# Optimization experiments

Measured on AMD Instinct MI355X. Metric: run time of the kernel, lower is better.

The kernel has to match this reference:

```python
import jax, jax.numpy as jnp
import numpy as np

V, E, H, S, B = 32000, 512, 1024, 32, 32


def setup_inputs() -> dict:
    key = jax.random.key(0)
    ks = jax.random.split(key, 16)
    s = 0.05
    return {
        "word": jax.random.randint(ks[0], (B,), 0, V),
        "seq": jax.random.randint(ks[1], (S, B), 0, V),
        "emb": jax.random.normal(ks[2], (V, E), jnp.float32) * s,
        "Wl": jax.random.normal(ks[3], (H, E), jnp.float32) * s,
        "bl": jnp.zeros((H,), jnp.float32),
        "Wih": jax.random.normal(ks[4], (4 * H, E), jnp.float32) * s,
        "Whh": jax.random.normal(ks[5], (4 * H, H), jnp.float32) * s,
        "bih": jnp.zeros((4 * H,), jnp.float32),
        "bhh": jnp.zeros((4 * H,), jnp.float32),
        "Wz": jax.random.normal(ks[6], (H, E + H), jnp.float32) * s,
        "bz": jnp.zeros((H,), jnp.float32),
        "Wr": jax.random.normal(ks[7], (E, E + H), jnp.float32) * s,
        "br": jnp.zeros((E,), jnp.float32),
        "Wh": jax.random.normal(ks[8], (H, E + H), jnp.float32) * s,
        "bh": jnp.zeros((H,), jnp.float32),
        "Wo": jax.random.normal(ks[9], (V, H), jnp.float32) * s,
        "bo": jnp.zeros((V,), jnp.float32),
    }


def reference(word, seq, emb, Wl, bl, Wih, Whh, bih, bhh, Wz, bz, Wr, br, Wh, bh, Wo, bo):
    we = emb[word]              # [B, E] defined-word embedding (constant per step)
    se = emb[seq]               # [S, B, E] definition token embeddings
    h0 = we @ Wl.T + bl         # word_linear init: hidden = (h0, h0)

    def step(carry, x):
        h, c = carry
        # torch LSTMCell: gate order i, f, g, o
        gates = x @ Wih.T + h @ Whh.T + (bih + bhh)
        i, f, g, o = jnp.split(gates, 4, axis=-1)
        c = jax.nn.sigmoid(f) * c + jax.nn.sigmoid(i) * jnp.tanh(g)
        h = jax.nn.sigmoid(o) * jnp.tanh(c)
        # GRU-style g-gating with the defined-word embedding
        inp_h = jnp.concatenate([we, h], axis=-1)           # [B, E+H]
        z = jax.nn.sigmoid(inp_h @ Wz.T + bz)               # [B, H]
        r = jax.nn.sigmoid(inp_h @ Wr.T + br)               # [B, E]
        hc = jnp.concatenate([r * we, h], axis=-1)          # [B, E+H]
        hh = jnp.tanh(hc @ Wh.T + bh)
        h = (1.0 - z) * h + z * hh
        return (h, c), h

    (hf, cf), hs = jax.lax.scan(step, (h0, h0), se)
    out = hs @ Wo.T + bo        # [S, B, V] logits (dropout p=0 -> identity)
    return out, hf, cf
```

## Files before the change

kernel.cpp:

```cpp
#include <hip/hip_runtime.h>


typedef __bf16 bf16;
typedef __bf16 bf16x8 __attribute__((ext_vector_type(8)));
typedef __bf16 bf16x4v __attribute__((ext_vector_type(4)));
typedef float f32x4 __attribute__((ext_vector_type(4)));
typedef unsigned long long u64;
typedef unsigned int u32;

#define Vv 32000
#define Ee 512
#define Hh 1024
#define Ss 32
#define Bb 32
#define KC 1536

#define MFMA16(a, b, c) __builtin_amdgcn_mfma_f32_16x16x32_bf16(a, b, c, 0, 0, 0)

static __device__ __forceinline__ float sigf(float x) { return 1.0f / (1.0f + __expf(-x)); }

static __device__ __forceinline__ u64 cload_u64(const void* p) {
  return __hip_atomic_load((const u64*)p, __ATOMIC_RELAXED, __HIP_MEMORY_SCOPE_SYSTEM);
}
static __device__ __forceinline__ void cstore_u64(void* p, u64 v) {
  __hip_atomic_store((u64*)p, v, __ATOMIC_RELAXED, __HIP_MEMORY_SCOPE_SYSTEM);
}
static __device__ __forceinline__ void cstore_u32(void* p, u32 v) {
  __hip_atomic_store((u32*)p, v, __ATOMIC_RELAXED, __HIP_MEMORY_SCOPE_SYSTEM);
}
static __device__ __forceinline__ bf16x8 cload_bf8(const bf16* p) {
  union { u64 w[2]; bf16x8 v; } u;
  u.w[0] = cload_u64(p);
  u.w[1] = cload_u64(p + 4);
  return u.v;
}
union F2U64 { float f[2]; u64 u; };
union B2U32 { bf16 h[2]; u32 u; };


__global__ void k_conv_gates(const float* __restrict__ Wih, const float* __restrict__ Whh,
                             const float* __restrict__ bih, const float* __restrict__ bhh,
                             bf16* __restrict__ Wgh, bf16* __restrict__ Wgl,
                             float* __restrict__ bg) {
  int g = blockIdx.y;
  int col = blockIdx.x * 256 + threadIdx.x;
  int k = g >> 2, s = g & 3;
  int src = s * Hh + k;
  float v = (col < Ee) ? Wih[(size_t)src * Ee + col] : Whh[(size_t)src * Hh + (col - Ee)];
  bf16 h = (bf16)v;
  Wgh[(size_t)g * KC + col] = h;
  Wgl[(size_t)g * KC + col] = (bf16)(v - (float)h);
  if (col == 0) bg[g] = bih[src] + bhh[src];
}

__global__ void k_conv_zr2(const float* __restrict__ Wz, const float* __restrict__ Wr,
                           bf16* __restrict__ W2h, bf16* __restrict__ W2l) {
  int j = blockIdx.y;
  int col = blockIdx.x * 256 + threadIdx.x;
  float v = (j < Hh) ? Wz[(size_t)j * KC + Ee + col] : Wr[(size_t)(j - Hh) * KC + Ee + col];
  bf16 h = (bf16)v;
  W2h[(size_t)j * Hh + col] = h;
  W2l[(size_t)j * Hh + col] = (bf16)(v - (float)h);
}

__global__ void k_conv_wh(const float* __restrict__ A, bf16* __restrict__ hi,
                          bf16* __restrict__ lo) {
  int j = blockIdx.y;
  int k = blockIdx.x * 256 + threadIdx.x;
  float v = A[(size_t)j * KC + k];
  bf16 h = (bf16)v;
  hi[(size_t)j * KC + k] = h;
  lo[(size_t)j * KC + k] = (bf16)(v - (float)h);
}


__global__ void k_gather_we(const int* __restrict__ word, const float* __restrict__ emb,
                            float* __restrict__ we) {
  int b = blockIdx.y;
  int e = blockIdx.x * 256 + threadIdx.x;
  we[b * Ee + e] = emb[(size_t)word[b] * Ee + e];
}

__global__ void k_gather_se(const int* __restrict__ seq, const float* __restrict__ emb,
                            bf16* __restrict__ se_h, bf16* __restrict__ se_l) {
  int tb = blockIdx.y;
  int e = blockIdx.x * 256 + threadIdx.x;
  float v = emb[(size_t)seq[tb] * Ee + e];
  bf16 h = (bf16)v;
  se_h[(size_t)tb * Ee + e] = h;
  se_l[(size_t)tb * Ee + e] = (bf16)(v - (float)h);
}

__global__ void k_init_h0(const float* __restrict__ we, const float* __restrict__ Wl,
                          const float* __restrict__ bl, float* __restrict__ c,
                          bf16* __restrict__ h_h, bf16* __restrict__ h_l) {
  int o = blockIdx.x * 4 + (threadIdx.x >> 6);
  int lane = threadIdx.x & 63;
  int b = o >> 10, n = o & 1023;
  const float* wr = we + b * Ee;
  const float* wl = Wl + (size_t)n * Ee;
  int e0 = lane * 8;
  float4 a0 = *(const float4*)(wr + e0);
  float4 a1 = *(const float4*)(wr + e0 + 4);
  float4 b0 = *(const float4*)(wl + e0);
  float4 b1 = *(const float4*)(wl + e0 + 4);
  float s = a0.x * b0.x + a0.y * b0.y + a0.z * b0.z + a0.w * b0.w +
            a1.x * b1.x + a1.y * b1.y + a1.z * b1.z + a1.w * b1.w;
  for (int off = 32; off; off >>= 1) s += __shfl_down(s, off);
  if (lane == 0) {
    s += bl[n];
    c[o] = s;
    bf16 h = (bf16)s;
    h_h[o] = h;
    h_l[o] = (bf16)(s - (float)h);
  }
}

__global__ __launch_bounds__(256) void k_zrwe(const float* __restrict__ we,
                                              const float* __restrict__ Wz,
                                              const float* __restrict__ Wr,
                                              const float* __restrict__ bz,
                                              const float* __restrict__ br,
                                              float* __restrict__ zrwe) {
  int tid = threadIdx.x;
  int w = tid >> 6, lane = tid & 63, l16 = lane & 15, quad = lane >> 4;
  int j0 = (blockIdx.x * 4 + w) * 16;
  int j = j0 + l16;
  const float* wrow = (j < Hh) ? (Wz + (size_t)j * KC) : (Wr + (size_t)(j - Hh) * KC);
  f32x4 acc[2];
  acc[0] = (f32x4){0.f, 0.f, 0.f, 0.f};
  acc[1] = (f32x4){0.f, 0.f, 0.f, 0.f};
  for (int kk = 0; kk < Ee; kk += 32) {
    bf16x8 bh, bl;
#pragma unroll
    for (int i = 0; i < 8; ++i) {
      float v = wrow[kk + quad * 8 + i];
      bf16 hv = (bf16)v;
      bh[i] = hv;
      bl[i] = (bf16)(v - (float)hv);
    }
#pragma unroll
    for (int mt = 0; mt < 2; ++mt) {
      bf16x8 ah, al;
      const float* arow = we + (size_t)(mt * 16 + l16) * Ee + kk + quad * 8;
#pragma unroll
      for (int i = 0; i < 8; ++i) {
        float v = arow[i];
        bf16 hv = (bf16)v;
        ah[i] = hv;
        al[i] = (bf16)(v - (float)hv);
      }
      acc[mt] = MFMA16(ah, bh, acc[mt]);
      acc[mt] = MFMA16(al, bh, acc[mt]);
      acc[mt] = MFMA16(ah, bl, acc[mt]);
    }
  }
  float bias = (j < Hh) ? bz[j] : br[j - Hh];
#pragma unroll
  for (int mt = 0; mt < 2; ++mt)
#pragma unroll
    for (int r = 0; r < 4; ++r) {
      int b = mt * 16 + quad * 4 + r;
      zrwe[b * KC + j] = acc[mt][r] + bias;
    }
}


struct RecurArgs {
  const bf16 *Wgh, *Wgl;
  const bf16 *W2h, *W2l;
  const bf16 *Whh2, *Whl2;
  const bf16 *seh, *sel;
  const float *bg;
  const float *bhb;
  const float *zrwe;
  const float *we;
  bf16 *h_h, *h_l;
  float *c, *hl, *z, *hf;
  bf16 *hlh, *hll;
  bf16 *rweh, *rwel;
  bf16 *hs;
  unsigned *bar;
};

static __device__ __forceinline__ void gridbar(unsigned* bar, unsigned n) {
  asm volatile("s_waitcnt vmcnt(0)" ::: "memory");
  __syncthreads();
  if (threadIdx.x == 0) {
    unsigned v = __hip_atomic_fetch_add(bar, 1u, __ATOMIC_RELAXED, __HIP_MEMORY_SCOPE_AGENT);
    if (v == n * 256u - 1u) {
      __hip_atomic_store(bar + 64, n, __ATOMIC_RELAXED, __HIP_MEMORY_SCOPE_AGENT);
    } else {
      while ((int)(__hip_atomic_fetch_add(bar + 64, 0u, __ATOMIC_RELAXED,
                                          __HIP_MEMORY_SCOPE_AGENT) -
                   n) < 0)
        __builtin_amdgcn_s_sleep(4);
    }
  }
  __syncthreads();
}

__global__ __launch_bounds__(512) void k_recur(RecurArgs a) {
  __shared__ __align__(16) bf16 sWa[2][16 * 1024];
  __shared__ __align__(16) bf16 sWx[2][16 * 1024];
  __shared__ float red[8][32][17];

  int blk = blockIdx.x, tid = threadIdx.x;
  int w = tid >> 6, lane = tid & 63, l16 = lane & 15, quad = lane >> 4;

  for (int i = tid; i < 2048; i += 512) {
    int row = i >> 7, ch = i & 127, e = ch * 8;
    int d = row * 1024 + (e ^ ((row & 7) << 3));
    *(bf16x8*)&sWa[0][d] = *(const bf16x8*)&a.Wgh[(size_t)(blk * 16 + row) * KC + Ee + e];
    *(bf16x8*)&sWa[1][d] = *(const bf16x8*)&a.Wgl[(size_t)(blk * 16 + row) * KC + Ee + e];
    if (blk < 96) {
      *(bf16x8*)&sWx[0][d] = *(const bf16x8*)&a.W2h[(size_t)(blk * 16 + row) * Hh + e];
      *(bf16x8*)&sWx[1][d] = *(const bf16x8*)&a.W2l[(size_t)(blk * 16 + row) * Hh + e];
    } else if (blk < 160) {
      *(bf16x8*)&sWx[0][d] =
          *(const bf16x8*)&a.Whh2[(size_t)((blk - 96) * 16 + row) * KC + Ee + e];
      *(bf16x8*)&sWx[1][d] =
          *(const bf16x8*)&a.Whl2[(size_t)((blk - 96) * 16 + row) * KC + Ee + e];
    }
  }
  __syncthreads();

  unsigned bcnt = 0;

  for (int t = 0; t < Ss; ++t) {
    {
      f32x4 acc[2];
      acc[0] = (f32x4){0.f, 0.f, 0.f, 0.f};
      acc[1] = (f32x4){0.f, 0.f, 0.f, 0.f};
#pragma unroll
      for (int it = 0; it < 6; ++it) {
        int kk = w * 192 + it * 32;
        bf16x8 bh, bl;
        if (kk < Ee) {
          bh = *(const bf16x8*)&a.Wgh[(size_t)(blk * 16 + l16) * KC + kk + quad * 8];
          bl = *(const bf16x8*)&a.Wgl[(size_t)(blk * 16 + l16) * KC + kk + quad * 8];
        } else {
          int eo = (kk - Ee) + quad * 8;
          int d = l16 * 1024 + (eo ^ ((l16 & 7) << 3));
          bh = *(const bf16x8*)&sWa[0][d];
          bl = *(const bf16x8*)&sWa[1][d];
        }
#pragma unroll
        for (int mt = 0; mt < 2; ++mt) {
          int bb = mt * 16 + l16;
          bf16x8 ah, al;
          if (kk < Ee) {
            ah = *(const bf16x8*)&a.seh[(size_t)(t * Bb + bb) * Ee + kk + quad * 8];
            al = *(const bf16x8*)&a.sel[(size_t)(t * Bb + bb) * Ee + kk + quad * 8];
          } else {
            ah = cload_bf8(&a.h_h[(size_t)bb * Hh + (kk - Ee) + quad * 8]);
            al = cload_bf8(&a.h_l[(size_t)bb * Hh + (kk - Ee) + quad * 8]);
          }
          acc[mt] = MFMA16(ah, bh, acc[mt]);
          acc[mt] = MFMA16(al, bh, acc[mt]);
          acc[mt] = MFMA16(ah, bl, acc[mt]);
        }
      }
#pragma unroll
      for (int mt = 0; mt < 2; ++mt)
#pragma unroll
        for (int r = 0; r < 4; ++r) red[w][mt * 16 + quad * 4 + r][l16] = acc[mt][r];
    }
    __syncthreads();
    if (tid < 64) {
      int bb = tid >> 1, kl0 = (tid & 1) * 2;
      B2U32 ph, pl;
      F2U64 phl;
#pragma unroll
      for (int u2 = 0; u2 < 2; ++u2) {
        int kl = kl0 + u2;
        float g4[4];
#pragma unroll
        for (int s = 0; s < 4; ++s) {
          int jl = kl * 4 + s;
          float sum = a.bg[blk * 16 + jl];
#pragma unroll
          for (int w2 = 0; w2 < 8; ++w2) sum += red[w2][bb][jl];
          g4[s] = sum;
        }
        int idx = bb * Hh + blk * 4 + kl;
        float cn = sigf(g4[1]) * a.c[idx] + sigf(g4[0]) * tanhf(g4[2]);
        float hvv = sigf(g4[3]) * tanhf(cn);
        a.c[idx] = cn;
        phl.f[u2] = hvv;
        bf16 hb = (bf16)hvv;
        ph.h[u2] = hb;
        pl.h[u2] = (bf16)(hvv - (float)hb);
      }
      int base = bb * Hh + blk * 4 + kl0;
      cstore_u64(&a.hl[base], phl.u);
      cstore_u32(&a.hlh[base], ph.u);
      cstore_u32(&a.hll[base], pl.u);
    }
    gridbar(a.bar, ++bcnt);

    if (blk < 96) {
      f32x4 acc[2];
      acc[0] = (f32x4){0.f, 0.f, 0.f, 0.f};
      acc[1] = (f32x4){0.f, 0.f, 0.f, 0.f};
#pragma unroll
      for (int it = 0; it < 4; ++it) {
        int kk = w * 128 + it * 32;
        int eo = kk + quad * 8;
        int d = l16 * 1024 + (eo ^ ((l16 & 7) << 3));
        bf16x8 bh = *(const bf16x8*)&sWx[0][d];
        bf16x8 bl = *(const bf16x8*)&sWx[1][d];
#pragma unroll
        for (int mt = 0; mt < 2; ++mt) {
          int bb = mt * 16 + l16;
          bf16x8 ah = cload_bf8(&a.hlh[(size_t)bb * Hh + kk + quad * 8]);
          bf16x8 al = cload_bf8(&a.hll[(size_t)bb * Hh + kk + quad * 8]);
          acc[mt] = MFMA16(ah, bh, acc[mt]);
          acc[mt] = MFMA16(al, bh, acc[mt]);
          acc[mt] = MFMA16(ah, bl, acc[mt]);
        }
      }
#pragma unroll
      for (int mt = 0; mt < 2; ++mt)
#pragma unroll
        for (int r = 0; r < 4; ++r) red[w][mt * 16 + quad * 4 + r][l16] = acc[mt][r];
      __syncthreads();
      if (tid < 256) {
        int bb = tid >> 3, jl0 = (tid & 7) * 2;
        float v[2];
#pragma unroll
        for (int u2 = 0; u2 < 2; ++u2) {
          int jl = jl0 + u2;
          int j = blk * 16 + jl;
          float s = a.zrwe[bb * KC + j];
#pragma unroll
          for (int w2 = 0; w2 < 8; ++w2) s += red[w2][bb][jl];
          v[u2] = s;
        }
        int j = blk * 16 + jl0;
        if (blk < 64) {
          F2U64 pz;
          pz.f[0] = sigf(v[0]);
          pz.f[1] = sigf(v[1]);
          cstore_u64(&a.z[bb * Hh + j], pz.u);
        } else {
          int e = j - Hh;
          B2U32 ph, pl;
#pragma unroll
          for (int u2 = 0; u2 < 2; ++u2) {
            float rv = sigf(v[u2]) * a.we[bb * Ee + e + u2];
            bf16 hb = (bf16)rv;
            ph.h[u2] = hb;
            pl.h[u2] = (bf16)(rv - (float)hb);
          }
          cstore_u32(&a.rweh[bb * Ee + e], ph.u);
          cstore_u32(&a.rwel[bb * Ee + e], pl.u);
        }
      }
    }
    gridbar(a.bar, ++bcnt);

    if (blk >= 96 && blk < 160) {
      int j0 = (blk - 96) * 16;
      f32x4 acc[2];
      acc[0] = (f32x4){0.f, 0.f, 0.f, 0.f};
      acc[1] = (f32x4){0.f, 0.f, 0.f, 0.f};
#pragma unroll
      for (int it = 0; it < 6; ++it) {
        int kk = w * 192 + it * 32;
        bf16x8 bh, bl;
        if (kk < Ee) {
          bh = *(const bf16x8*)&a.Whh2[(size_t)(j0 + l16) * KC + kk + quad * 8];
          bl = *(const bf16x8*)&a.Whl2[(size_t)(j0 + l16) * KC + kk + quad * 8];
        } else {
          int eo = (kk - Ee) + quad * 8;
          int d = l16 * 1024 + (eo ^ ((l16 & 7) << 3));
          bh = *(const bf16x8*)&sWx[0][d];
          bl = *(const bf16x8*)&sWx[1][d];
        }
#pragma unroll
        for (int mt = 0; mt < 2; ++mt) {
          int bb = mt * 16 + l16;
          bf16x8 ah, al;
          if (kk < Ee) {
            ah = cload_bf8(&a.rweh[(size_t)bb * Ee + kk + quad * 8]);
            al = cload_bf8(&a.rwel[(size_t)bb * Ee + kk + quad * 8]);
          } else {
            ah = cload_bf8(&a.hlh[(size_t)bb * Hh + (kk - Ee) + quad * 8]);
            al = cload_bf8(&a.hll[(size_t)bb * Hh + (kk - Ee) + quad * 8]);
          }
          acc[mt] = MFMA16(ah, bh, acc[mt]);
          acc[mt] = MFMA16(al, bh, acc[mt]);
          acc[mt] = MFMA16(ah, bl, acc[mt]);
        }
      }
#pragma unroll
      for (int mt = 0; mt < 2; ++mt)
#pragma unroll
        for (int r = 0; r < 4; ++r) red[w][mt * 16 + quad * 4 + r][l16] = acc[mt][r];
      __syncthreads();
      if (tid < 256) {
        int bb = tid >> 3, jl0 = (tid & 7) * 2;
        int j = j0 + jl0;
        F2U64 hlp, zp;
        hlp.u = cload_u64(&a.hl[bb * Hh + j]);
        zp.u = cload_u64(&a.z[bb * Hh + j]);
        B2U32 ph, pl, phs;
        float hf2[2];
#pragma unroll
        for (int u2 = 0; u2 < 2; ++u2) {
          int jl = jl0 + u2;
          float s = a.bhb[j + u2];
#pragma unroll
          for (int w2 = 0; w2 < 8; ++w2) s += red[w2][bb][jl];
          float hhv = tanhf(s);
          float hn = (1.f - zp.f[u2]) * hlp.f[u2] + zp.f[u2] * hhv;
          hf2[u2] = hn;
          bf16 hb = (bf16)hn;
          ph.h[u2] = hb;
          pl.h[u2] = (bf16)(hn - (float)hb);
          phs.h[u2] = hb;
        }
        a.hf[bb * Hh + j] = hf2[0];
        a.hf[bb * Hh + j + 1] = hf2[1];
        cstore_u32(&a.h_h[bb * Hh + j], ph.u);
        cstore_u32(&a.h_l[bb * Hh + j], pl.u);
        *(u32*)&a.hs[((size_t)t * Bb + bb) * Hh + j] = phs.u;
      }
    }
    gridbar(a.bar, ++bcnt);
  }
}


__global__ __launch_bounds__(256) void k_gemm_out(const bf16* __restrict__ hs,
                                                  const float* __restrict__ Wo,
                                                  const float* __restrict__ bo,
                                                  float* __restrict__ out) {
  int id = blockIdx.x;
  int r_ = id & 7, s_ = id >> 3;
  int mi = s_ & 7;
  int ni = (s_ >> 3) * 8 + r_;
  if (ni >= Vv / 128) return;
  int m0 = mi * 128, n0 = ni * 128;

  int tid = threadIdx.x;
  int w = tid >> 6, lane = tid & 63;
  int l16 = lane & 15, quad = lane >> 4;
  int wm = w & 1, wn = w >> 1;
  int swl = ((l16 >> 1) & 3) << 3;

  __shared__ __align__(16) bf16 A_lds[128 * 32];
  __shared__ __align__(16) bf16 B_lds[128 * 32];

  f32x4 acc[4][4];
#pragma unroll
  for (int i = 0; i < 4; ++i)
#pragma unroll
    for (int j = 0; j < 4; ++j) acc[i][j] = (f32x4){0.f, 0.f, 0.f, 0.f};

  for (int kt = 0; kt < 32; ++kt) {
    int k0 = kt * 32;
#pragma unroll
    for (int i = 0; i < 2; ++i) {
      int cid = tid + i * 256;
      int row = cid >> 2, ch = cid & 3;
      int sw = ((row >> 1) & 3) << 3;
      *(int4*)&A_lds[row * 32 + ((ch * 8) ^ sw)] =
          *(const int4*)&hs[(size_t)(m0 + row) * Hh + k0 + ch * 8];
    }
#pragma unroll
    for (int i = 0; i < 4; ++i) {
      int cid = tid + i * 256;
      int row = cid >> 3, ch = cid & 7;
      int sw = ((row >> 1) & 3) << 3;
      float4 v = *(const float4*)&Wo[(size_t)(n0 + row) * Hh + k0 + ch * 4];
      bf16x4v bv = {(bf16)v.x, (bf16)v.y, (bf16)v.z, (bf16)v.w};
      *(bf16x4v*)&B_lds[row * 32 + ((ch * 4) ^ sw)] = bv;
    }
    __syncthreads();

    bf16x8 af[4], bfr[4];
#pragma unroll
    for (int i = 0; i < 4; ++i)
      af[i] = *(const bf16x8*)&A_lds[(wm * 64 + i * 16 + l16) * 32 + ((quad * 8) ^ swl)];
#pragma unroll
    for (int j = 0; j < 4; ++j)
      bfr[j] = *(const bf16x8*)&B_lds[(wn * 64 + j * 16 + l16) * 32 + ((quad * 8) ^ swl)];
#pragma unroll
    for (int i = 0; i < 4; ++i)
#pragma unroll
      for (int j = 0; j < 4; ++j) acc[i][j] = MFMA16(af[i], bfr[j], acc[i][j]);
    __syncthreads();
  }

#pragma unroll
  for (int i = 0; i < 4; ++i)
#pragma unroll
    for (int j = 0; j < 4; ++j)
#pragma unroll
      for (int r = 0; r < 4; ++r) {
        int m = m0 + wm * 64 + i * 16 + quad * 4 + r;
        int n = n0 + wn * 64 + j * 16 + l16;
        out[(size_t)m * Vv + n] = acc[i][j][r] + bo[n];
      }
}

__global__ void k_copy_hc(const float* __restrict__ h_f32, const float* __restrict__ c_f32,
                          float* __restrict__ out) {
  int i = blockIdx.x * 256 + threadIdx.x;
  size_t base = (size_t)Ss * Bb * Vv;
  out[base + i] = h_f32[i];
  out[base + Bb * Hh + i] = c_f32[i];
}


extern "C" void kernel_launch(void* const* d_in, const int* in_sizes, int n_in,
                              void* d_out, int out_size, void* d_ws, size_t ws_size,
                              hipStream_t stream) {
  const int* word = (const int*)d_in[0];
  const int* seq = (const int*)d_in[1];
  const float* emb = (const float*)d_in[2];
  const float* Wl = (const float*)d_in[3];
  const float* bl = (const float*)d_in[4];
  const float* Wih = (const float*)d_in[5];
  const float* Whh = (const float*)d_in[6];
  const float* bih = (const float*)d_in[7];
  const float* bhh = (const float*)d_in[8];
  const float* Wz = (const float*)d_in[9];
  const float* bz = (const float*)d_in[10];
  const float* Wr = (const float*)d_in[11];
  const float* br = (const float*)d_in[12];
  const float* Wh = (const float*)d_in[13];
  const float* bh = (const float*)d_in[14];
  const float* Wo = (const float*)d_in[15];
  const float* bo = (const float*)d_in[16];
  float* out = (float*)d_out;

  char* p = (char*)d_ws;
  auto alloc = [&](size_t bytes) -> char* {
    char* q = p;
    p += (bytes + 255) & ~(size_t)255;
    return q;
  };
  unsigned* bar = (unsigned*)alloc(1024);
  float* we_f32 = (float*)alloc(Bb * Ee * 4);
  float* zrwe = (float*)alloc(Bb * KC * 4);
  float* c_f32 = (float*)alloc(Bb * Hh * 4);
  float* hl_f32 = (float*)alloc(Bb * Hh * 4);
  float* z_f32 = (float*)alloc(Bb * Hh * 4);
  float* hf_f32 = (float*)alloc(Bb * Hh * 4);
  bf16* h_h = (bf16*)alloc(Bb * Hh * 2);
  bf16* h_l = (bf16*)alloc(Bb * Hh * 2);
  bf16* hlh = (bf16*)alloc(Bb * Hh * 2);
  bf16* hll = (bf16*)alloc(Bb * Hh * 2);
  bf16* rweh = (bf16*)alloc(Bb * Ee * 2);
  bf16* rwel = (bf16*)alloc(Bb * Ee * 2);
  bf16* se_h = (bf16*)alloc((size_t)Ss * Bb * Ee * 2);
  bf16* se_l = (bf16*)alloc((size_t)Ss * Bb * Ee * 2);
  bf16* hs_b = (bf16*)alloc((size_t)Ss * Bb * Hh * 2);
  bf16* Wgh = (bf16*)alloc((size_t)4 * Hh * KC * 2);
  bf16* Wgl = (bf16*)alloc((size_t)4 * Hh * KC * 2);
  bf16* W2h = (bf16*)alloc((size_t)KC * Hh * 2);
  bf16* W2l = (bf16*)alloc((size_t)KC * Hh * 2);
  bf16* Whh2 = (bf16*)alloc((size_t)Hh * KC * 2);
  bf16* Whl2 = (bf16*)alloc((size_t)Hh * KC * 2);
  float* bg = (float*)alloc((size_t)4 * Hh * 4);

  dim3 blk(256);
  hipMemsetAsync(bar, 0, 1024, stream);
  k_conv_gates<<<dim3(6, 4096), blk, 0, stream>>>(Wih, Whh, bih, bhh, Wgh, Wgl, bg);
  k_conv_zr2<<<dim3(4, 1536), blk, 0, stream>>>(Wz, Wr, W2h, W2l);
  k_conv_wh<<<dim3(6, 1024), blk, 0, stream>>>(Wh, Whh2, Whl2);
  k_gather_we<<<dim3(2, 32), blk, 0, stream>>>(word, emb, we_f32);
  k_gather_se<<<dim3(2, Ss * Bb), blk, 0, stream>>>(seq, emb, se_h, se_l);
  k_init_h0<<<8192, blk, 0, stream>>>(we_f32, Wl, bl, c_f32, h_h, h_l);
  k_zrwe<<<24, blk, 0, stream>>>(we_f32, Wz, Wr, bz, br, zrwe);

  RecurArgs ra;
  ra.Wgh = Wgh; ra.Wgl = Wgl;
  ra.W2h = W2h; ra.W2l = W2l;
  ra.Whh2 = Whh2; ra.Whl2 = Whl2;
  ra.seh = se_h; ra.sel = se_l;
  ra.bg = bg; ra.bhb = bh; ra.zrwe = zrwe; ra.we = we_f32;
  ra.h_h = h_h; ra.h_l = h_l;
  ra.c = c_f32; ra.hl = hl_f32; ra.z = z_f32; ra.hf = hf_f32;
  ra.hlh = hlh; ra.hll = hll;
  ra.rweh = rweh; ra.rwel = rwel;
  ra.hs = hs_b;
  ra.bar = bar;
  k_recur<<<256, dim3(512), 0, stream>>>(ra);

  k_gemm_out<<<2048, blk, 0, stream>>>(hs_b, Wo, bo, out);
  k_copy_hc<<<128, blk, 0, stream>>>(hf_f32, c_f32, out);
}
```

Measured before the change: 1.853 ms.

## Replace flat grid barrier with hierarchical producer-subset barriers and double-buffer output GEMM

The single all-block grid barrier, used three times per step, is replaced with a two-level arrive/wait barrier. Only the blocks that produce data for a phase arrive, and only the blocks that consume it wait, so idle blocks skip intermediate barriers and the contention on one counter is spread across per-group counters. Separately, the output projection GEMM now double-buffers LDS and prefetches the next K tile into registers while the MFMAs run. The barrier change removes the trailing s_waitcnt vmcnt(0) fence, which risks memory-visibility bugs that rely on relaxed atomics. It also uses more barrier memory.

```diff
diff --git a/kernel.cpp b/kernel.cpp
--- a/kernel.cpp
+++ b/kernel.cpp
@@ -36,6 +36,28 @@
 }
 union F2U64 { float f[2]; u64 u; };
 union B2U32 { bf16 h[2]; u32 u; };
+
+static __device__ __forceinline__ void bar_arrive(u32* bar, int cntOff, int rootOff, int genOff,
+                                                  u32 grpSize, u32 nGrp, int g, u32 t1) {
+  __syncthreads();
+  if (threadIdx.x == 0) {
+    u32 v = __hip_atomic_fetch_add(bar + cntOff + g * 32, 1u, __ATOMIC_RELAXED,
+                                   __HIP_MEMORY_SCOPE_AGENT);
+    if (v == grpSize * t1 - 1u) {
+      u32 r = __hip_atomic_fetch_add(bar + rootOff, 1u, __ATOMIC_RELAXED,
+                                     __HIP_MEMORY_SCOPE_AGENT);
+      if (r == nGrp * t1 - 1u)
+        __hip_atomic_store(bar + genOff, t1, __ATOMIC_RELAXED, __HIP_MEMORY_SCOPE_SYSTEM);
+    }
+  }
+}
+static __device__ __forceinline__ void bar_wait(u32* bar, int genOff, u32 t1) {
+  if (threadIdx.x == 0) {
+    while (__hip_atomic_load(bar + genOff, __ATOMIC_RELAXED, __HIP_MEMORY_SCOPE_SYSTEM) < t1)
+      __builtin_amdgcn_s_sleep(8);
+  }
+  __syncthreads();
+}
 
 
 __global__ void k_conv_gates(const float* __restrict__ Wih, const float* __restrict__ Whh,
@@ -183,23 +205,6 @@
   unsigned *bar;
 };
 
-static __device__ __forceinline__ void gridbar(unsigned* bar, unsigned n) {
-  asm volatile("s_waitcnt vmcnt(0)" ::: "memory");
-  __syncthreads();
-  if (threadIdx.x == 0) {
-    unsigned v = __hip_atomic_fetch_add(bar, 1u, __ATOMIC_RELAXED, __HIP_MEMORY_SCOPE_AGENT);
-    if (v == n * 256u - 1u) {
-      __hip_atomic_store(bar + 64, n, __ATOMIC_RELAXED, __HIP_MEMORY_SCOPE_AGENT);
-    } else {
-      while ((int)(__hip_atomic_fetch_add(bar + 64, 0u, __ATOMIC_RELAXED,
-                                          __HIP_MEMORY_SCOPE_AGENT) -
-                   n) < 0)
-        __builtin_amdgcn_s_sleep(4);
-    }
-  }
-  __syncthreads();
-}
-
 __global__ __launch_bounds__(512) void k_recur(RecurArgs a) {
   __shared__ __align__(16) bf16 sWa[2][16 * 1024];
   __shared__ __align__(16) bf16 sWx[2][16 * 1024];
@@ -225,9 +230,8 @@
   }
   __syncthreads();
 
-  unsigned bcnt = 0;
-
   for (int t = 0; t < Ss; ++t) {
+    u32 t1 = (u32)(t + 1);
     {
       f32x4 acc[2];
       acc[0] = (f32x4){0.f, 0.f, 0.f, 0.f};
@@ -297,9 +301,10 @@
       cstore_u32(&a.hlh[base], ph.u);
       cstore_u32(&a.hll[base], pl.u);
     }
-    gridbar(a.bar, ++bcnt);
+    bar_arrive(a.bar, 0, 256, 288, 32, 8, blk >> 5, t1);
 
     if (blk < 96) {
+      bar_wait(a.bar, 288, t1);
       f32x4 acc[2];
       acc[0] = (f32x4){0.f, 0.f, 0.f, 0.f};
       acc[1] = (f32x4){0.f, 0.f, 0.f, 0.f};
@@ -357,10 +362,9 @@
           cstore_u32(&a.rwel[bb * Ee + e], pl.u);
         }
       }
-    }
-    gridbar(a.bar, ++bcnt);
-
-    if (blk >= 96 && blk < 160) {
+      bar_arrive(a.bar, 320, 512, 544, 16, 6, blk >> 4, t1);
+    } else if (blk < 160) {
+      bar_wait(a.bar, 544, t1);
       int j0 = (blk - 96) * 16;
       f32x4 acc[2];
       acc[0] = (f32x4){0.f, 0.f, 0.f, 0.f};
@@ -427,8 +431,9 @@
         cstore_u32(&a.h_l[bb * Hh + j], pl.u);
         *(u32*)&a.hs[((size_t)t * Bb + bb) * Hh + j] = phs.u;
       }
-    }
-    gridbar(a.bar, ++bcnt);
+      bar_arrive(a.bar, 576, 832, 864, 8, 8, (blk - 96) >> 3, t1);
+    }
+    bar_wait(a.bar, 864, t1);
   }
 }
 
@@ -450,8 +455,8 @@
   int wm = w & 1, wn = w >> 1;
   int swl = ((l16 >> 1) & 3) << 3;
 
-  __shared__ __align__(16) bf16 A_lds[128 * 32];
-  __shared__ __align__(16) bf16 B_lds[128 * 32];
+  __shared__ __align__(16) bf16 A_lds[2][128 * 32];
+  __shared__ __align__(16) bf16 B_lds[2][128 * 32];
 
   f32x4 acc[4][4];
 #pragma unroll
@@ -459,39 +464,64 @@
 #pragma unroll
     for (int j = 0; j < 4; ++j) acc[i][j] = (f32x4){0.f, 0.f, 0.f, 0.f};
 
-  for (int kt = 0; kt < 32; ++kt) {
+  int4 ra[2];
+  float4 rb[4];
+  auto LOADR = [&](int kt) {
     int k0 = kt * 32;
+#pragma unroll
+    for (int i = 0; i < 2; ++i) {
+      int cid = tid + i * 256;
+      int row = cid >> 2, ch = cid & 3;
+      ra[i] = *(const int4*)&hs[(size_t)(m0 + row) * Hh + k0 + ch * 8];
+    }
+#pragma unroll
+    for (int i = 0; i < 4; ++i) {
+      int cid = tid + i * 256;
+      int row = cid >> 3, ch = cid & 7;
+      rb[i] = *(const float4*)&Wo[(size_t)(n0 + row) * Hh + k0 + ch * 4];
+    }
+  };
+  auto STORELDS = [&](int buf) {
 #pragma unroll
     for (int i = 0; i < 2; ++i) {
       int cid = tid + i * 256;
       int row = cid >> 2, ch = cid & 3;
       int sw = ((row >> 1) & 3) << 3;
-      *(int4*)&A_lds[row * 32 + ((ch * 8) ^ sw)] =
-          *(const int4*)&hs[(size_t)(m0 + row) * Hh + k0 + ch * 8];
+      *(int4*)&A_lds[buf][row * 32 + ((ch * 8) ^ sw)] = ra[i];
     }
 #pragma unroll
     for (int i = 0; i < 4; ++i) {
       int cid = tid + i * 256;
       int row = cid >> 3, ch = cid & 7;
       int sw = ((row >> 1) & 3) << 3;
-      float4 v = *(const float4*)&Wo[(size_t)(n0 + row) * Hh + k0 + ch * 4];
+      float4 v = rb[i];
       bf16x4v bv = {(bf16)v.x, (bf16)v.y, (bf16)v.z, (bf16)v.w};
-      *(bf16x4v*)&B_lds[row * 32 + ((ch * 4) ^ sw)] = bv;
-    }
-    __syncthreads();
-
+      *(bf16x4v*)&B_lds[buf][row * 32 + ((ch * 4) ^ sw)] = bv;
+    }
+  };
+
+  LOADR(0);
+  STORELDS(0);
+  __syncthreads();
+  int cur = 0;
+  for (int kt = 0; kt < 32; ++kt) {
+    if (kt < 31) LOADR(kt + 1);
     bf16x8 af[4], bfr[4];
 #pragma unroll
     for (int i = 0; i < 4; ++i)
-      af[i] = *(const bf16x8*)&A_lds[(wm * 64 + i * 16 + l16) * 32 + ((quad * 8) ^ swl)];
+      af[i] = *(const bf16x8*)&A_lds[cur][(wm * 64 + i * 16 + l16) * 32 + ((quad * 8) ^ swl)];
 #pragma unroll
     for (int j = 0; j < 4; ++j)
-      bfr[j] = *(const bf16x8*)&B_lds[(wn * 64 + j * 16 + l16) * 32 + ((quad * 8) ^ swl)];
+      bfr[j] = *(const bf16x8*)&B_lds[cur][(wn * 64 + j * 16 + l16) * 32 + ((quad * 8) ^ swl)];
 #pragma unroll
     for (int i = 0; i < 4; ++i)
 #pragma unroll
       for (int j = 0; j < 4; ++j) acc[i][j] = MFMA16(af[i], bfr[j], acc[i][j]);
-    __syncthreads();
+    if (kt < 31) {
+      STORELDS(cur ^ 1);
+      __syncthreads();
+      cur ^= 1;
+    }
   }
 
 #pragma unroll
@@ -543,7 +573,7 @@
     p += (bytes + 255) & ~(size_t)255;
     return q;
   };
-  unsigned* bar = (unsigned*)alloc(1024);
+  unsigned* bar = (unsigned*)alloc(4096);
   float* we_f32 = (float*)alloc(Bb * Ee * 4);
   float* zrwe = (float*)alloc(Bb * KC * 4);
   float* c_f32 = (float*)alloc(Bb * Hh * 4);
@@ -568,7 +598,7 @@
   float* bg = (float*)alloc((size_t)4 * Hh * 4);
 
   dim3 blk(256);
-  hipMemsetAsync(bar, 0, 1024, stream);
+  hipMemsetAsync(bar, 0, 4096, stream);
   k_conv_gates<<<dim3(6, 4096), blk, 0, stream>>>(Wih, Whh, bih, bhh, Wgh, Wgl, bg);
   k_conv_zr2<<<dim3(4, 1536), blk, 0, stream>>>(Wz, Wr, W2h, W2l);
   k_conv_wh<<<dim3(6, 1024), blk, 0, stream>>>(Wh, Whh2, Whl2);
```

After: 1.798 ms. 3.0% less time.
